# Performance work log

Hardware: AMD Instinct MI355X
Metric: run time of the kernel (lower is better)

The kernel has to match this reference:

```python
import jax, jax.numpy as jnp
import numpy as np

B, M, F_N, D, GS, L = 32, 512, 64, 128, 4, 8  # batch, max atoms, in feats, int_d, graph channels, layers


def setup_inputs() -> dict:
    key = jax.random.key(0)
    ks = jax.random.split(key, 8)
    G = jax.random.uniform(ks[0], (B, GS, M, M), dtype=jnp.float32)      # dense multi-channel adjacency
    x = jax.random.normal(ks[1], (B, M, F_N), dtype=jnp.float32)          # per-atom features
    W0 = jax.random.normal(ks[2], (GS, F_N, D), dtype=jnp.float32) * 0.05 # per-channel Linear, layer 0
    b0 = jax.random.normal(ks[3], (GS, D), dtype=jnp.float32) * 0.05
    Wl = jax.random.normal(ks[4], (L - 1, GS, D, D), dtype=jnp.float32) * 0.05
    bl = jax.random.normal(ks[5], (L - 1, GS, D), dtype=jnp.float32) * 0.05
    Wout = jax.random.normal(ks[6], (D, 1), dtype=jnp.float32) * 0.05
    bout = jax.random.normal(ks[7], (1,), dtype=jnp.float32) * 0.05
    return {"G": G, "x": x, "W0": W0, "b0": b0, "Wl": Wl, "bl": bl, "Wout": Wout, "bout": bout}


def _graph_mat_layer(G, h, W, b):
    # per-channel linear: [B,M,C] x [GS,C,P] -> [B,GS,M,P]
    multi = jnp.einsum('bmc,gcp->bgmp', h, W) + b[None, :, None, :]
    # per-sample, per-channel adjacency matmul: [B,GS,M,M] @ [B,GS,M,P]
    xout = jnp.einsum('bgmn,bgnp->bgmp', G, multi)
    # ReLU then goodmax aggregation over graph channels (dim=1)
    return jnp.max(jax.nn.relu(xout), axis=1)  # [B,M,P]


def reference(G, x, W0, b0, Wl, bl, Wout, bout):
    # layer 0: input width F_N != D, so no residual (shape mismatch)
    h = _graph_mat_layer(G, x, W0, b0)
    # layers 1..L-1: resnet skip (shapes match)
    for i in range(L - 1):
        h = _graph_mat_layer(G, h, Wl[i], bl[i]) + h
    # lin_out on [B,M,D] -> [B,M,1]
    return h @ Wout + bout
```

## Files before the change

### kernel.cpp

```cpp
#include <hip/hip_runtime.h>
#include <stdint.h>


#define B_  32
#define M_  512
#define FN_ 64
#define D_  128
#define GS_ 4
#define L_  8

typedef __attribute__((ext_vector_type(8))) short short8;
typedef __attribute__((ext_vector_type(4))) float f32x4;
typedef unsigned short us;

__device__ __forceinline__ us f2bf(float f) {
  union { float f; unsigned int u; } v; v.f = f;
  return (us)((v.u + 0x7FFFu + ((v.u >> 16) & 1u)) >> 16);
}

__device__ __forceinline__ void gl16(const void* g, void* l) {
  __builtin_amdgcn_global_load_lds((const __attribute__((address_space(1))) void*)g,
                                   (__attribute__((address_space(3))) void*)l, 16, 0, 0);
}

__global__ void k_conv(const float4* __restrict__ src, ushort4* __restrict__ dst, int n4) {
  int i = blockIdx.x * blockDim.x + threadIdx.x;
  int st = gridDim.x * blockDim.x;
  for (; i < n4; i += st) {
    float4 v = src[i];
    ushort4 o;
    o.x = f2bf(v.x); o.y = f2bf(v.y); o.z = f2bf(v.z); o.w = f2bf(v.w);
    dst[i] = o;
  }
}

__global__ void k_convW(const float* __restrict__ W0, const float* __restrict__ Wl,
                        us* __restrict__ W0bT, us* __restrict__ WlbT) {
  int i = blockIdx.x * blockDim.x + threadIdx.x;
  const int n0 = GS_ * FN_ * D_;
  if (i < n0) {
    int g = i / (FN_ * D_), r = i % (FN_ * D_), c = r / D_, p = r % D_;
    W0bT[((size_t)g * D_ + p) * FN_ + c] = f2bf(W0[i]);
  } else {
    int j = i - n0;
    if (j < 7 * GS_ * D_ * D_) {
      int l = j / (GS_ * D_ * D_), r = j % (GS_ * D_ * D_);
      int g = r / (D_ * D_), r2 = r % (D_ * D_), c = r2 / D_, p = r2 % D_;
      WlbT[(((size_t)l * GS_ + g) * D_ + p) * D_ + c] = f2bf(Wl[j]);
    }
  }
}

template<int NK>
__launch_bounds__(256)
__global__ void k_lin(const us* __restrict__ A0, const us* __restrict__ B0,
                      int aRS, int aSB, int bSG,
                      us* __restrict__ outBf, const float* __restrict__ bias) {
  __shared__ __align__(16) us sm[2][2][4096];
  const int t = threadIdx.x;
  const int bid = blockIdx.x;
  const int mt = bid & 3, g = (bid >> 2) & 3, b = bid >> 4;
  const us* Ap = A0 + (size_t)b * aSB + (size_t)mt * 128 * aRS;
  const us* Bp = B0 + (size_t)g * bSG;

  const int tr = t >> 2;
  const int tc = (t & 3) * 8;

  {
    const us* ga = Ap + (size_t)tr * aRS + tc;
    const us* gb = Bp + (size_t)tr * aRS + tc;
    gl16(ga, &sm[0][0][t * 8]);
    gl16(ga + (size_t)64 * aRS, &sm[0][0][2048 + t * 8]);
    gl16(gb, &sm[0][1][t * 8]);
    gl16(gb + (size_t)64 * aRS, &sm[0][1][2048 + t * 8]);
  }

  const int lane = t & 63;
  const int wm = ((t >> 7) & 1) * 64;
  const int wp = ((t >> 6) & 1) * 64;
  const int lr = lane & 15;
  const int lk = (lane >> 4) * 8;

  f32x4 acc[4][4];
#pragma unroll
  for (int i = 0; i < 4; ++i)
#pragma unroll
    for (int j = 0; j < 4; ++j) acc[i][j] = (f32x4){0.f, 0.f, 0.f, 0.f};

  int cur = 0;
  for (int ks = 0; ks < NK; ++ks) {
    __syncthreads();
    if (ks + 1 < NK) {
      const int nb = cur ^ 1;
      const us* ga = Ap + (size_t)(ks + 1) * 32 + (size_t)tr * aRS + tc;
      const us* gb = Bp + (size_t)(ks + 1) * 32 + (size_t)tr * aRS + tc;
      gl16(ga, &sm[nb][0][t * 8]);
      gl16(ga + (size_t)64 * aRS, &sm[nb][0][2048 + t * 8]);
      gl16(gb, &sm[nb][1][t * 8]);
      gl16(gb + (size_t)64 * aRS, &sm[nb][1][2048 + t * 8]);
    }
    const us* sa = sm[cur][0];
    const us* sb = sm[cur][1];
    short8 af[4], bfr[4];
#pragma unroll
    for (int i = 0; i < 4; ++i)
      af[i] = *(const short8*)&sa[(wm + i * 16 + lr) * 32 + lk];
#pragma unroll
    for (int j = 0; j < 4; ++j)
      bfr[j] = *(const short8*)&sb[(wp + j * 16 + lr) * 32 + lk];
#pragma unroll
    for (int i = 0; i < 4; ++i)
#pragma unroll
      for (int j = 0; j < 4; ++j)
        acc[i][j] = __builtin_amdgcn_mfma_f32_16x16x32_bf16(af[i], bfr[j], acc[i][j], 0, 0, 0);
    cur ^= 1;
  }

  const int rb = (lane >> 4) * 4;
#pragma unroll
  for (int j = 0; j < 4; ++j) {
    const int p = wp + j * 16 + lr;
    const float bv = bias[g * D_ + p];
    us* op = outBf + ((size_t)(b * GS_ + g) * D_ + p) * M_;
#pragma unroll
    for (int i = 0; i < 4; ++i) {
      const int n = mt * 128 + wm + i * 16 + rb;
      f32x4 v = acc[i][j];
      ushort4 o;
      o.x = f2bf(v[0] + bv); o.y = f2bf(v[1] + bv);
      o.z = f2bf(v[2] + bv); o.w = f2bf(v[3] + bv);
      *(ushort4*)(op + n) = o;
    }
  }
}

template<int FIRST>
__launch_bounds__(512, 2)
__global__ void k_fused(const us* __restrict__ Gh, const us* __restrict__ MhT,
                        float* __restrict__ h, us* __restrict__ hb) {
  __shared__ __align__(16) us sm[65536];
  const int bid = blockIdx.x;
  const int swz = (bid & 7) * 32 + (bid >> 3);
  const int b = swz >> 3, mt = swz & 7;

  const int t = threadIdx.x;
  const int w = t >> 6;
  const int g = w >> 1;
  const int wp = (w & 1) * 64;
  const int lane = t & 63;
  const int lr = lane & 15;
  const int kq = lane >> 4;

  const us* AgB = Gh + ((size_t)(b * GS_ + g) * M_ + mt * 64) * M_;
  const us* BgB = MhT + ((size_t)(b * GS_ + g) * D_ + wp) * M_;
  const int aoff = (lane >> 2) * M_ + (lane & 3) * 8;
  us* smW = sm + w * 8192;

#define STG(c, ks) do { \
    const us* ga_ = AgB + (ks) * 32 + aoff; \
    const us* gb_ = BgB + (ks) * 32 + aoff; \
    us* ld_ = smW + (c) * 4096 + lane * 8; \
    gl16(ga_,              ld_); \
    gl16(ga_ + 16 * M_,    ld_ + 512); \
    gl16(ga_ + 32 * M_,    ld_ + 1024); \
    gl16(ga_ + 48 * M_,    ld_ + 1536); \
    gl16(gb_,              ld_ + 2048); \
    gl16(gb_ + 16 * M_,    ld_ + 2560); \
    gl16(gb_ + 32 * M_,    ld_ + 3072); \
    gl16(gb_ + 48 * M_,    ld_ + 3584); \
  } while (0)

  f32x4 acc[4][4];
#pragma unroll
  for (int i = 0; i < 4; ++i)
#pragma unroll
    for (int j = 0; j < 4; ++j) acc[i][j] = (f32x4){0.f, 0.f, 0.f, 0.f};

  STG(0, 0);

  const int fo = lr * 32 + kq * 8;
#pragma unroll 2
  for (int ks = 0; ks < 16; ++ks) {
    const int cur = ks & 1;
    asm volatile("s_waitcnt lgkmcnt(0)" ::: "memory");
    if (ks < 15) {
      STG(cur ^ 1, ks + 1);
      asm volatile("s_waitcnt vmcnt(8)" ::: "memory");
    } else {
      asm volatile("s_waitcnt vmcnt(0)" ::: "memory");
    }
    const us* sa = smW + cur * 4096;
    const us* sb = sa + 2048;
    short8 af[4], bf[4];
#pragma unroll
    for (int i = 0; i < 4; ++i) af[i] = *(const short8*)&sa[i * 512 + fo];
#pragma unroll
    for (int j = 0; j < 4; ++j) bf[j] = *(const short8*)&sb[j * 512 + fo];
#pragma unroll
    for (int i = 0; i < 4; ++i)
#pragma unroll
      for (int j = 0; j < 4; ++j)
        acc[i][j] = __builtin_amdgcn_mfma_f32_16x16x32_bf16(af[i], bf[j], acc[i][j], 0, 0, 0);
  }
#undef STG

  __syncthreads();

  {
    float* red = (float*)sm + (size_t)g * 8192;
    const int rb = kq * 4;
#pragma unroll
    for (int i = 0; i < 4; ++i)
#pragma unroll
      for (int j = 0; j < 4; ++j) {
        float* cp = red + (size_t)(i * 16 + rb) * D_ + wp + j * 16 + lr;
        cp[0]      = fmaxf(acc[i][j][0], 0.f);
        cp[D_]     = fmaxf(acc[i][j][1], 0.f);
        cp[2 * D_] = fmaxf(acc[i][j][2], 0.f);
        cp[3 * D_] = fmaxf(acc[i][j][3], 0.f);
      }
  }
  __syncthreads();

  {
    const int m_l = t >> 3, p0 = (t & 7) * 16;
    const float* r0 = (float*)sm + (size_t)m_l * D_ + p0;
    float4 vm[4];
#pragma unroll
    for (int k = 0; k < 4; ++k) vm[k] = ((const float4*)r0)[k];
#pragma unroll
    for (int gg = 1; gg < 4; ++gg) {
      const float4* rg = (const float4*)(r0 + (size_t)gg * 8192);
#pragma unroll
      for (int k = 0; k < 4; ++k) {
        float4 u = rg[k];
        vm[k].x = fmaxf(vm[k].x, u.x); vm[k].y = fmaxf(vm[k].y, u.y);
        vm[k].z = fmaxf(vm[k].z, u.z); vm[k].w = fmaxf(vm[k].w, u.w);
      }
    }
    const size_t ho = ((size_t)b * M_ + mt * 64 + m_l) * D_ + p0;
    float4* hp = (float4*)(h + ho);
    ushort4* hbp = (ushort4*)(hb + ho);
#pragma unroll
    for (int k = 0; k < 4; ++k) {
      float4 v = vm[k];
      if (!FIRST) {
        float4 hv = hp[k];
        v.x += hv.x; v.y += hv.y; v.z += hv.z; v.w += hv.w;
      }
      hp[k] = v;
      ushort4 o;
      o.x = f2bf(v.x); o.y = f2bf(v.y); o.z = f2bf(v.z); o.w = f2bf(v.w);
      hp[k] = v;
      hbp[k] = o;
    }
  }
}

__global__ void k_out(const float* __restrict__ h, const float* __restrict__ Wout,
                      const float* __restrict__ bout, float* __restrict__ out) {
  const int w = blockIdx.x * 4 + (threadIdx.x >> 6);
  const int lane = threadIdx.x & 63;
  const float2 hv = ((const float2*)(h + (size_t)w * D_))[lane];
  const float2 wv = ((const float2*)Wout)[lane];
  float s = hv.x * wv.x + hv.y * wv.y;
#pragma unroll
  for (int o = 32; o; o >>= 1) s += __shfl_down(s, o);
  if (lane == 0) out[w] = s + bout[0];
}

extern "C" void kernel_launch(void* const* d_in, const int* in_sizes, int n_in,
                              void* d_out, int out_size, void* d_ws, size_t ws_size,
                              hipStream_t stream) {
  const float* G    = (const float*)d_in[0];
  const float* x    = (const float*)d_in[1];
  const float* W0   = (const float*)d_in[2];
  const float* b0   = (const float*)d_in[3];
  const float* Wl   = (const float*)d_in[4];
  const float* bl   = (const float*)d_in[5];
  const float* Wout = (const float*)d_in[6];
  const float* bout = (const float*)d_in[7];

  char* ws = (char*)d_ws;
  us*    Gh   = (us*)(ws);
  us*    MhT  = (us*)(ws + 67108864);
  float* h    = (float*)(ws + 83886080);
  us*    hb   = (us*)(ws + 92274688);
  us*    xb   = (us*)(ws + 96468992);
  us*    W0bT = (us*)(ws + 98566144);
  us*    WlbT = (us*)(ws + 98631680);

  k_conv<<<2048, 256, 0, stream>>>((const float4*)G, (ushort4*)Gh, (B_ * GS_ * M_ * M_) / 4);
  k_conv<<<1024, 256, 0, stream>>>((const float4*)x, (ushort4*)xb, (B_ * M_ * FN_) / 4);
  k_convW<<<1920, 256, 0, stream>>>(W0, Wl, W0bT, WlbT);

  k_lin<FN_ / 32><<<512, 256, 0, stream>>>(xb, W0bT, FN_, M_ * FN_, D_ * FN_, MhT, b0);
  k_fused<1><<<256, 512, 0, stream>>>(Gh, MhT, h, hb);

  for (int l = 1; l < L_; ++l) {
    k_lin<D_ / 32><<<512, 256, 0, stream>>>(hb, WlbT + (size_t)(l - 1) * GS_ * D_ * D_,
        D_, M_ * D_, D_ * D_, MhT, bl + (size_t)(l - 1) * GS_ * D_);
    k_fused<0><<<256, 512, 0, stream>>>(Gh, MhT, h, hb);
  }

  k_out<<<4096, 256, 0, stream>>>(h, Wout, bout, (float*)d_out);
}
```

Baseline: 317.7 us.

## Share MhT tiles across wave pairs, triple-buffer fused GEMM, swizzle LDS, fuse output head

The fused adjacency GEMM now stages each channel's A and B tiles once into a buffer shared by the two waves of that channel, instead of one private copy per wave. Loading runs through a three-deep ring with block barriers, so fetches run two steps ahead. LDS layouts in k_lin, the fused kernel and the reduction buffer get XOR swizzles to avoid bank conflicts. The last layer computes the output projection in-kernel via shuffle reductions, removing the separate k_out launch and the final h/hb writes. The cost is an extra block-wide barrier in every k-step and more LDS per block, which may lower occupancy.

```diff
diff --git a/kernel.cpp b/kernel.cpp
--- a/kernel.cpp
+++ b/kernel.cpp
@@ -64,11 +64,11 @@
   const us* Bp = B0 + (size_t)g * bSG;
 
   const int tr = t >> 2;
-  const int tc = (t & 3) * 8;
+  const int tcs = ((t & 3) ^ ((t >> 3) & 3)) * 8;
 
   {
-    const us* ga = Ap + (size_t)tr * aRS + tc;
-    const us* gb = Bp + (size_t)tr * aRS + tc;
+    const us* ga = Ap + (size_t)tr * aRS + tcs;
+    const us* gb = Bp + (size_t)tr * aRS + tcs;
     gl16(ga, &sm[0][0][t * 8]);
     gl16(ga + (size_t)64 * aRS, &sm[0][0][2048 + t * 8]);
     gl16(gb, &sm[0][1][t * 8]);
@@ -79,7 +79,7 @@
   const int wm = ((t >> 7) & 1) * 64;
   const int wp = ((t >> 6) & 1) * 64;
   const int lr = lane & 15;
-  const int lk = (lane >> 4) * 8;
+  const int kk = (((lane >> 4) ^ ((lane >> 1) & 3))) * 8;
 
   f32x4 acc[4][4];
 #pragma unroll
@@ -92,8 +92,8 @@
     __syncthreads();
     if (ks + 1 < NK) {
       const int nb = cur ^ 1;
-      const us* ga = Ap + (size_t)(ks + 1) * 32 + (size_t)tr * aRS + tc;
-      const us* gb = Bp + (size_t)(ks + 1) * 32 + (size_t)tr * aRS + tc;
+      const us* ga = Ap + (size_t)(ks + 1) * 32 + (size_t)tr * aRS + tcs;
+      const us* gb = Bp + (size_t)(ks + 1) * 32 + (size_t)tr * aRS + tcs;
       gl16(ga, &sm[nb][0][t * 8]);
       gl16(ga + (size_t)64 * aRS, &sm[nb][0][2048 + t * 8]);
       gl16(gb, &sm[nb][1][t * 8]);
@@ -104,10 +104,10 @@
     short8 af[4], bfr[4];
 #pragma unroll
     for (int i = 0; i < 4; ++i)
-      af[i] = *(const short8*)&sa[(wm + i * 16 + lr) * 32 + lk];
+      af[i] = *(const short8*)&sa[(wm + i * 16 + lr) * 32 + kk];
 #pragma unroll
     for (int j = 0; j < 4; ++j)
-      bfr[j] = *(const short8*)&sb[(wp + j * 16 + lr) * 32 + lk];
+      bfr[j] = *(const short8*)&sb[(wp + j * 16 + lr) * 32 + kk];
 #pragma unroll
     for (int i = 0; i < 4; ++i)
 #pragma unroll
@@ -134,11 +134,13 @@
   }
 }
 
-template<int FIRST>
+template<int FIRST, int LAST>
 __launch_bounds__(512, 2)
 __global__ void k_fused(const us* __restrict__ Gh, const us* __restrict__ MhT,
-                        float* __restrict__ h, us* __restrict__ hb) {
-  __shared__ __align__(16) us sm[65536];
+                        float* __restrict__ h, us* __restrict__ hb,
+                        const float* __restrict__ Wout, const float* __restrict__ bout,
+                        float* __restrict__ out) {
+  __shared__ __align__(16) us sm[3 * 24576];
   const int bid = blockIdx.x;
   const int swz = (bid & 7) * 32 + (bid >> 3);
   const int b = swz >> 3, mt = swz & 7;
@@ -146,28 +148,27 @@
   const int t = threadIdx.x;
   const int w = t >> 6;
   const int g = w >> 1;
-  const int wp = (w & 1) * 64;
+  const int hf = w & 1;
   const int lane = t & 63;
   const int lr = lane & 15;
   const int kq = lane >> 4;
 
   const us* AgB = Gh + ((size_t)(b * GS_ + g) * M_ + mt * 64) * M_;
-  const us* BgB = MhT + ((size_t)(b * GS_ + g) * D_ + wp) * M_;
-  const int aoff = (lane >> 2) * M_ + (lane & 3) * 8;
-  us* smW = sm + w * 8192;
-
-#define STG(c, ks) do { \
-    const us* ga_ = AgB + (ks) * 32 + aoff; \
-    const us* gb_ = BgB + (ks) * 32 + aoff; \
-    us* ld_ = smW + (c) * 4096 + lane * 8; \
-    gl16(ga_,              ld_); \
-    gl16(ga_ + 16 * M_,    ld_ + 512); \
-    gl16(ga_ + 32 * M_,    ld_ + 1024); \
-    gl16(ga_ + 48 * M_,    ld_ + 1536); \
-    gl16(gb_,              ld_ + 2048); \
-    gl16(gb_ + 16 * M_,    ld_ + 2560); \
-    gl16(gb_ + 32 * M_,    ld_ + 3072); \
-    gl16(gb_ + 48 * M_,    ld_ + 3584); \
+  const us* BgB = MhT + (size_t)(b * GS_ + g) * D_ * M_;
+  const int srow = lane >> 2;
+  const int scol = ((lane & 3) ^ ((lane >> 3) & 3)) * 8;
+  const int s0 = hf * 6;
+
+#define STAGE(bufi, ks) do { \
+    us* bb_ = sm + (bufi) * 24576 + g * 6144; \
+    _Pragma("unroll") \
+    for (int u_ = 0; u_ < 6; ++u_) { \
+      const int ls_ = s0 + u_; \
+      const us* src_ = (ls_ < 4) \
+        ? AgB + (size_t)(ls_ * 16 + srow) * M_ + (ks) * 32 + scol \
+        : BgB + (size_t)((ls_ - 4) * 16 + srow) * M_ + (ks) * 32 + scol; \
+      gl16(src_, bb_ + ls_ * 512 + lane * 8); \
+    } \
   } while (0)
 
   f32x4 acc[4][4];
@@ -176,97 +177,107 @@
 #pragma unroll
     for (int j = 0; j < 4; ++j) acc[i][j] = (f32x4){0.f, 0.f, 0.f, 0.f};
 
-  STG(0, 0);
-
-  const int fo = lr * 32 + kq * 8;
-#pragma unroll 2
+  STAGE(0, 0);
+  STAGE(1, 1);
+
+  const int kk = ((kq ^ ((lr >> 1) & 3))) * 8;
+
+#pragma unroll
   for (int ks = 0; ks < 16; ++ks) {
-    const int cur = ks & 1;
-    asm volatile("s_waitcnt lgkmcnt(0)" ::: "memory");
-    if (ks < 15) {
-      STG(cur ^ 1, ks + 1);
-      asm volatile("s_waitcnt vmcnt(8)" ::: "memory");
-    } else {
-      asm volatile("s_waitcnt vmcnt(0)" ::: "memory");
-    }
-    const us* sa = smW + cur * 4096;
+    if (ks < 15) asm volatile("s_waitcnt vmcnt(6)" ::: "memory");
+    else         asm volatile("s_waitcnt vmcnt(0)" ::: "memory");
+    __builtin_amdgcn_s_barrier();
+    __builtin_amdgcn_sched_barrier(0);
+    const us* sa = sm + (ks % 3) * 24576 + g * 6144;
     const us* sb = sa + 2048;
     short8 af[4], bf[4];
 #pragma unroll
-    for (int i = 0; i < 4; ++i) af[i] = *(const short8*)&sa[i * 512 + fo];
-#pragma unroll
-    for (int j = 0; j < 4; ++j) bf[j] = *(const short8*)&sb[j * 512 + fo];
+    for (int i = 0; i < 4; ++i)
+      af[i] = *(const short8*)&sa[(i * 16 + lr) * 32 + kk];
+#pragma unroll
+    for (int j = 0; j < 4; ++j)
+      bf[j] = *(const short8*)&sb[(hf * 64 + j * 16 + lr) * 32 + kk];
+    if (ks + 2 < 16) STAGE((ks + 2) % 3, ks + 2);
+    asm volatile("s_waitcnt lgkmcnt(0)" ::: "memory");
+    __builtin_amdgcn_sched_barrier(0);
 #pragma unroll
     for (int i = 0; i < 4; ++i)
 #pragma unroll
       for (int j = 0; j < 4; ++j)
         acc[i][j] = __builtin_amdgcn_mfma_f32_16x16x32_bf16(af[i], bf[j], acc[i][j], 0, 0, 0);
   }
-#undef STG
-
-  __syncthreads();
+#undef STAGE
+
+  __builtin_amdgcn_s_barrier();
+  __builtin_amdgcn_sched_barrier(0);
 
   {
     float* red = (float*)sm + (size_t)g * 8192;
-    const int rb = kq * 4;
 #pragma unroll
     for (int i = 0; i < 4; ++i)
 #pragma unroll
       for (int j = 0; j < 4; ++j) {
-        float* cp = red + (size_t)(i * 16 + rb) * D_ + wp + j * 16 + lr;
-        cp[0]      = fmaxf(acc[i][j][0], 0.f);
-        cp[D_]     = fmaxf(acc[i][j][1], 0.f);
-        cp[2 * D_] = fmaxf(acc[i][j][2], 0.f);
-        cp[3 * D_] = fmaxf(acc[i][j][3], 0.f);
-      }
-  }
-  __syncthreads();
+        const int col = hf * 64 + j * 16 + lr;
+        const int ch = col >> 2, cw = col & 3;
+#pragma unroll
+        for (int cc = 0; cc < 4; ++cc) {
+          const int row = i * 16 + kq * 4 + cc;
+          red[row * 128 + ((ch ^ (row & 7)) << 2) + cw] = fmaxf(acc[i][j][cc], 0.f);
+        }
+      }
+  }
+  __builtin_amdgcn_s_barrier();
+  __builtin_amdgcn_sched_barrier(0);
 
   {
-    const int m_l = t >> 3, p0 = (t & 7) * 16;
-    const float* r0 = (float*)sm + (size_t)m_l * D_ + p0;
+    const int m_l = t >> 3, pq = t & 7;
+    const float* red = (const float*)sm;
     float4 vm[4];
 #pragma unroll
-    for (int k = 0; k < 4; ++k) vm[k] = ((const float4*)r0)[k];
-#pragma unroll
-    for (int gg = 1; gg < 4; ++gg) {
-      const float4* rg = (const float4*)(r0 + (size_t)gg * 8192);
+    for (int k = 0; k < 4; ++k) {
+      const int ch = pq * 4 + k;
+      const float* rp = red + (size_t)m_l * 128 + ((ch ^ (m_l & 7)) << 2);
+      float4 v = *(const float4*)rp;
+#pragma unroll
+      for (int gg = 1; gg < 4; ++gg) {
+        float4 u = *(const float4*)(rp + (size_t)gg * 8192);
+        v.x = fmaxf(v.x, u.x); v.y = fmaxf(v.y, u.y);
+        v.z = fmaxf(v.z, u.z); v.w = fmaxf(v.w, u.w);
+      }
+      vm[k] = v;
+    }
+    const size_t ho = ((size_t)b * M_ + mt * 64 + m_l) * D_ + pq * 16;
+    float4* hp = (float4*)(h + ho);
+    if (!FIRST) {
 #pragma unroll
       for (int k = 0; k < 4; ++k) {
-        float4 u = rg[k];
-        vm[k].x = fmaxf(vm[k].x, u.x); vm[k].y = fmaxf(vm[k].y, u.y);
-        vm[k].z = fmaxf(vm[k].z, u.z); vm[k].w = fmaxf(vm[k].w, u.w);
-      }
-    }
-    const size_t ho = ((size_t)b * M_ + mt * 64 + m_l) * D_ + p0;
-    float4* hp = (float4*)(h + ho);
-    ushort4* hbp = (ushort4*)(hb + ho);
-#pragma unroll
-    for (int k = 0; k < 4; ++k) {
-      float4 v = vm[k];
-      if (!FIRST) {
         float4 hv = hp[k];
-        v.x += hv.x; v.y += hv.y; v.z += hv.z; v.w += hv.w;
-      }
-      hp[k] = v;
-      ushort4 o;
-      o.x = f2bf(v.x); o.y = f2bf(v.y); o.z = f2bf(v.z); o.w = f2bf(v.w);
-      hp[k] = v;
-      hbp[k] = o;
-    }
-  }
-}
-
-__global__ void k_out(const float* __restrict__ h, const float* __restrict__ Wout,
-                      const float* __restrict__ bout, float* __restrict__ out) {
-  const int w = blockIdx.x * 4 + (threadIdx.x >> 6);
-  const int lane = threadIdx.x & 63;
-  const float2 hv = ((const float2*)(h + (size_t)w * D_))[lane];
-  const float2 wv = ((const float2*)Wout)[lane];
-  float s = hv.x * wv.x + hv.y * wv.y;
-#pragma unroll
-  for (int o = 32; o; o >>= 1) s += __shfl_down(s, o);
-  if (lane == 0) out[w] = s + bout[0];
+        vm[k].x += hv.x; vm[k].y += hv.y; vm[k].z += hv.z; vm[k].w += hv.w;
+      }
+    }
+    if constexpr (!LAST) {
+      ushort4* hbp = (ushort4*)(hb + ho);
+#pragma unroll
+      for (int k = 0; k < 4; ++k) {
+        float4 v = vm[k];
+        hp[k] = v;
+        ushort4 o;
+        o.x = f2bf(v.x); o.y = f2bf(v.y); o.z = f2bf(v.z); o.w = f2bf(v.w);
+        hbp[k] = o;
+      }
+    } else {
+      float s = 0.f;
+#pragma unroll
+      for (int k = 0; k < 4; ++k) {
+        const float4 wv = *(const float4*)(Wout + pq * 16 + k * 4);
+        s += vm[k].x * wv.x + vm[k].y * wv.y + vm[k].z * wv.z + vm[k].w * wv.w;
+      }
+      s += __shfl_xor(s, 1);
+      s += __shfl_xor(s, 2);
+      s += __shfl_xor(s, 4);
+      if (pq == 0) out[(size_t)b * M_ + mt * 64 + m_l] = s + bout[0];
+    }
+  }
 }
 
 extern "C" void kernel_launch(void* const* d_in, const int* in_sizes, int n_in,
@@ -295,13 +306,15 @@
   k_convW<<<1920, 256, 0, stream>>>(W0, Wl, W0bT, WlbT);
 
   k_lin<FN_ / 32><<<512, 256, 0, stream>>>(xb, W0bT, FN_, M_ * FN_, D_ * FN_, MhT, b0);
-  k_fused<1><<<256, 512, 0, stream>>>(Gh, MhT, h, hb);
-
-  for (int l = 1; l < L_; ++l) {
+  k_fused<1, 0><<<256, 512, 0, stream>>>(Gh, MhT, h, hb, Wout, bout, (float*)d_out);
+
+  for (int l = 1; l < L_ - 1; ++l) {
     k_lin<D_ / 32><<<512, 256, 0, stream>>>(hb, WlbT + (size_t)(l - 1) * GS_ * D_ * D_,
         D_, M_ * D_, D_ * D_, MhT, bl + (size_t)(l - 1) * GS_ * D_);
-    k_fused<0><<<256, 512, 0, stream>>>(Gh, MhT, h, hb);
-  }
-
-  k_out<<<4096, 256, 0, stream>>>(h, Wout, bout, (float*)d_out);
-}
+    k_fused<0, 0><<<256, 512, 0, stream>>>(Gh, MhT, h, hb, Wout, bout, (float*)d_out);
+  }
+
+  k_lin<D_ / 32><<<512, 256, 0, stream>>>(hb, WlbT + (size_t)(L_ - 2) * GS_ * D_ * D_,
+      D_, M_ * D_, D_ * D_, MhT, bl + (size_t)(L_ - 2) * GS_ * D_);
+  k_fused<0, 1><<<256, 512, 0, stream>>>(Gh, MhT, h, hb, Wout, bout, (float*)d_out);
+}
```

New measurement: 314.3 us. Within noise of the previous version (-1.1%).
